# Performance work log

Hardware: AMD Instinct MI355X
Metric: run time of the kernel (lower is better)

## Reference

```python
import jax, jax.numpy as jnp
import numpy as np

N = 50000
E = 800000
NUM_GRAPHS = 64

def gat_layer(x, W, att_src, att_dst, bias, src, dst, heads, out_ch, concat):
    n = x.shape[0]
    h = (x @ W).reshape(n, heads, out_ch)                      # [N,H,C]
    a_s = jnp.sum(h * att_src, axis=-1)                        # [N,H]
    a_d = jnp.sum(h * att_dst, axis=-1)                        # [N,H]
    e = jax.nn.leaky_relu(a_s[src] + a_d[dst], 0.2)            # [E,H]
    m = jax.ops.segment_max(e, dst, num_segments=n)            # segment softmax (self-loops guarantee non-empty)
    e = jnp.exp(e - m[dst])
    s = jax.ops.segment_sum(e, dst, num_segments=n)
    alpha = e / s[dst]                                         # [E,H]
    out = jax.ops.segment_sum(alpha[:, :, None] * h[src], dst, num_segments=n)  # [N,H,C]
    out = out.reshape(n, heads * out_ch) if concat else out.mean(axis=1)
    return out + bias

def setup_inputs() -> dict:
    key = jax.random.key(0)
    ks = jax.random.split(key, 20)
    inp = {}
    inp['x'] = jax.random.normal(ks[0], (N, 256), dtype=jnp.float32)
    inp['edge_index'] = jax.random.randint(ks[1], (2, E), 0, N, dtype=jnp.int64)
    inp['batch'] = jnp.sort(jax.random.randint(ks[2], (N,), 0, NUM_GRAPHS, dtype=jnp.int64))
    s = 0.05
    inp['W1'] = jax.random.normal(ks[3], (256, 256), dtype=jnp.float32) * s
    inp['att_src1'] = jax.random.normal(ks[4], (8, 32), dtype=jnp.float32) * s
    inp['att_dst1'] = jax.random.normal(ks[5], (8, 32), dtype=jnp.float32) * s
    inp['b1'] = jax.random.normal(ks[6], (256,), dtype=jnp.float32) * s
    inp['W2'] = jax.random.normal(ks[7], (256, 256), dtype=jnp.float32) * s
    inp['att_src2'] = jax.random.normal(ks[8], (8, 32), dtype=jnp.float32) * s
    inp['att_dst2'] = jax.random.normal(ks[9], (8, 32), dtype=jnp.float32) * s
    inp['b2'] = jax.random.normal(ks[10], (256,), dtype=jnp.float32) * s
    inp['W3'] = jax.random.normal(ks[11], (256, 32), dtype=jnp.float32) * s
    inp['att_src3'] = jax.random.normal(ks[12], (1, 32), dtype=jnp.float32) * s
    inp['att_dst3'] = jax.random.normal(ks[13], (1, 32), dtype=jnp.float32) * s
    inp['b3'] = jax.random.normal(ks[14], (32,), dtype=jnp.float32) * s
    inp['linW'] = jax.random.normal(ks[15], (32, 1), dtype=jnp.float32) * s
    inp['linb'] = jax.random.normal(ks[16], (1,), dtype=jnp.float32) * s
    return inp

def reference(x, edge_index, batch, W1, att_src1, att_dst1, b1, W2, att_src2, att_dst2, b2,
              W3, att_src3, att_dst3, b3, linW, linb):
    # add self loops (PyG add_self_loops=True)
    loop = jnp.arange(N, dtype=edge_index.dtype)
    src = jnp.concatenate([edge_index[0], loop])
    dst = jnp.concatenate([edge_index[1], loop])
    # eval mode: dropout is identity
    h = gat_layer(x, W1, att_src1, att_dst1, b1, src, dst, 8, 32, True)
    h = jax.nn.elu(h)
    h = gat_layer(h, W2, att_src2, att_dst2, b2, src, dst, 8, 32, True)
    h = jax.nn.elu(h)
    h = gat_layer(h, W3, att_src3, att_dst3, b3, src, dst, 1, 32, False)
    # global mean pool over all nodes (topic_mask defaults to all True)
    sums = jax.ops.segment_sum(h, batch, num_segments=NUM_GRAPHS)
    cnts = jax.ops.segment_sum(jnp.ones((N,), h.dtype), batch, num_segments=NUM_GRAPHS)
    pooled = sums / jnp.maximum(cnts, 1.0)[:, None]
    out = pooled @ linW + linb                                  # [G,1]
    return out.squeeze(-1)                                      # num_classes==2
```

## Files before the change

### kernel.cpp

```cpp
#include <hip/hip_runtime.h>
#include <hip/hip_fp8.h>
#include <math.h>


typedef __attribute__((ext_vector_type(8))) __bf16 bf16x8;
typedef __attribute__((ext_vector_type(4))) __bf16 bf16x4;
typedef __attribute__((ext_vector_type(4))) float f32x4;
typedef __attribute__((ext_vector_type(2))) float f32x2;

#define SCAN_CH 4

__device__ inline unsigned char f32_to_fp8(float f) {
  __hip_fp8_e4m3 v(f);
  return (unsigned char)v.__x;
}
__device__ inline float fp8_to_f32(unsigned char u) {
  __hip_fp8_e4m3 v;
  v.__x = (__hip_fp8_storage_t)u;
  return (float)v;
}

__device__ inline void fma_fp8x4(f32x4& acc, float w, unsigned int packed) {
#if defined(__has_builtin) && __has_builtin(__builtin_amdgcn_cvt_pk_f32_fp8)
  f32x2 lo = __builtin_amdgcn_cvt_pk_f32_fp8((int)packed, false);
  f32x2 hi = __builtin_amdgcn_cvt_pk_f32_fp8((int)packed, true);
  acc[0] += w * lo[0];
  acc[1] += w * lo[1];
  acc[2] += w * hi[0];
  acc[3] += w * hi[1];
#else
  acc[0] += w * fp8_to_f32((unsigned char)(packed & 0xff));
  acc[1] += w * fp8_to_f32((unsigned char)((packed >> 8) & 0xff));
  acc[2] += w * fp8_to_f32((unsigned char)((packed >> 16) & 0xff));
  acc[3] += w * fp8_to_f32((unsigned char)(packed >> 24));
#endif
}

__global__ __launch_bounds__(256) void k_init_deg(int* deg, int N) {
  int n = blockIdx.x * 256 + threadIdx.x;
  if (n < N) deg[n] = 1;
}

__global__ __launch_bounds__(256) void k_count_deg(const int* __restrict__ ei,
                                                   int E, int* deg) {
  int e = blockIdx.x * 256 + threadIdx.x;
  if (e < E) atomicAdd(&deg[ei[E + e]], 1);
}

__global__ __launch_bounds__(256) void k_scan_partial(const int* __restrict__ deg,
                                                      int* __restrict__ blockSums,
                                                      int N) {
  __shared__ int sh[256];
  int t = threadIdx.x, b = blockIdx.x;
  int base = (b * 256 + t) * SCAN_CH;
  int s = 0;
#pragma unroll
  for (int j = 0; j < SCAN_CH; j++) {
    int idx = base + j;
    if (idx < N) s += deg[idx];
  }
  sh[t] = s;
  __syncthreads();
  for (int off = 128; off > 0; off >>= 1) {
    if (t < off) sh[t] += sh[t + off];
    __syncthreads();
  }
  if (t == 0) blockSums[b] = sh[0];
}

__global__ __launch_bounds__(256) void k_scan_blocksums(
    const int* __restrict__ blockSums, int* __restrict__ blockOffs,
    int* __restrict__ rowptr, int nb, int N) {
  __shared__ int sh[256];
  int t = threadIdx.x;
  int v = (t < nb) ? blockSums[t] : 0;
  sh[t] = v;
  __syncthreads();
  for (int off = 1; off < 256; off <<= 1) {
    int u = (t >= off) ? sh[t - off] : 0;
    __syncthreads();
    sh[t] += u;
    __syncthreads();
  }
  if (t < nb) blockOffs[t] = sh[t] - v;
  if (t == nb - 1) rowptr[N] = sh[t];
}

__global__ __launch_bounds__(256) void k_scan_final(const int* __restrict__ deg,
                                                    const int* __restrict__ blockOffs,
                                                    int* __restrict__ rowptr,
                                                    int* __restrict__ cursor, int N) {
  __shared__ int sh[256];
  int t = threadIdx.x, b = blockIdx.x;
  int base = (b * 256 + t) * SCAN_CH;
  int vals[SCAN_CH];
  int s = 0;
#pragma unroll
  for (int j = 0; j < SCAN_CH; j++) {
    int idx = base + j;
    vals[j] = (idx < N) ? deg[idx] : 0;
    s += vals[j];
  }
  sh[t] = s;
  __syncthreads();
  for (int off = 1; off < 256; off <<= 1) {
    int u = (t >= off) ? sh[t - off] : 0;
    __syncthreads();
    sh[t] += u;
    __syncthreads();
  }
  int run = blockOffs[b] + sh[t] - s;
#pragma unroll
  for (int j = 0; j < SCAN_CH; j++) {
    int idx = base + j;
    if (idx < N) {
      rowptr[idx] = run;
      cursor[idx] = run;
      run += vals[j];
    }
  }
}

__global__ __launch_bounds__(256) void k_scatter2(const int* __restrict__ ei,
                                                  int E, int N, int* cursor,
                                                  int2* __restrict__ col2,
                                                  int chunkSz) {
  int stripe = blockIdx.x & 7;
  int chunk = blockIdx.x >> 3;
  int lo = (int)(((long long)N * stripe) >> 3);
  int hi = (int)(((long long)N * (stripe + 1)) >> 3);
  int base = chunk * chunkSz;
  int end = base + chunkSz;
  int total = E + N;
  if (end > total) end = total;
  for (int i = base + threadIdx.x; i < end; i += 256) {
    int d = (i < E) ? ei[E + i] : (i - E);
    if (d < lo || d >= hi) continue;
    int s = (i < E) ? ei[i] : d;
    int pos = atomicAdd(&cursor[d], 1);
    col2[pos] = make_int2(s, d);
  }
}

__global__ __launch_bounds__(256) void k_cast(const float* __restrict__ in,
                                              __bf16* __restrict__ oh, int n4) {
  int i = blockIdx.x * 256 + threadIdx.x;
  if (i >= n4) return;
  float4 v = ((const float4*)in)[i];
  bf16x4 h;
  h[0] = (__bf16)v.x;
  h[1] = (__bf16)v.y;
  h[2] = (__bf16)v.z;
  h[3] = (__bf16)v.w;
  ((bf16x4*)oh)[i] = h;
}

__global__ __launch_bounds__(256) void k_wprep(const float* __restrict__ W,
                                               __bf16* __restrict__ WTh,
                                               int K, int Nc) {
  int i = blockIdx.x * 256 + threadIdx.x;
  if (i >= K * Nc) return;
  int n = i / K, k = i - n * K;
  WTh[i] = (__bf16)W[k * Nc + n];
}

__global__ __launch_bounds__(256) void k_gemm_sA(
    const __bf16* __restrict__ Ah, const __bf16* __restrict__ BTh,
    __bf16* __restrict__ Ch, unsigned char* __restrict__ Cf8, int M, int K) {
  constexpr int NcFull = 256;
  __shared__ __bf16 sA[64 * 256];
  int tid = threadIdx.x;
  int lane = tid & 63, wave = tid >> 6;
  int quad = lane >> 4, l16 = lane & 15;
  int m0 = blockIdx.x * 64;
  int col0 = wave * 64;
  int srow = tid >> 2;
  int mtw = srow >> 4, l16w = srow & 15;
  int arow = min(m0 + srow, M - 1);
  const __bf16* ag = Ah + (size_t)arow * K;
#pragma unroll
  for (int r = 0; r < 8; r++) {
    int c = (tid & 3) + r * 4;
    int s = c >> 2, q = c & 3;
    int slot = (((s * 4 + mtw) * 4 + q) * 16 + l16w) * 8;
    *(bf16x8*)(sA + slot) = *(const bf16x8*)(ag + c * 8);
  }
  __syncthreads();
  const __bf16* brh = BTh + (size_t)(col0 + l16) * K + quad * 8;
  f32x4 acc[4][4];
#pragma unroll
  for (int mt = 0; mt < 4; mt++)
#pragma unroll
    for (int t = 0; t < 4; t++) acc[mt][t] = (f32x4){0.f, 0.f, 0.f, 0.f};
  for (int s = 0; s < 8; s++) {
    bf16x8 b_h[4];
#pragma unroll
    for (int t = 0; t < 4; t++)
      b_h[t] = *(const bf16x8*)(brh + (size_t)t * 16 * K + s * 32);
    bf16x8 a_h[4];
#pragma unroll
    for (int mt = 0; mt < 4; mt++)
      a_h[mt] = *(const bf16x8*)(sA + (((s * 4 + mt) * 4 + quad) * 16 + l16) * 8);
#pragma unroll
    for (int t = 0; t < 4; t++) {
#pragma unroll
      for (int mt = 0; mt < 4; mt++) {
        acc[mt][t] = __builtin_amdgcn_mfma_f32_16x16x32_bf16(a_h[mt], b_h[t], acc[mt][t], 0, 0, 0);
      }
    }
  }
#pragma unroll
  for (int mt = 0; mt < 4; mt++) {
#pragma unroll
    for (int t = 0; t < 4; t++) {
#pragma unroll
      for (int r = 0; r < 4; r++) {
        int m = m0 + mt * 16 + quad * 4 + r;
        if (m < M) {
          size_t o = (size_t)m * NcFull + col0 + t * 16 + l16;
          Ch[o] = (__bf16)acc[mt][t][r];
          Cf8[o] = f32_to_fp8(acc[mt][t][r]);
        }
      }
    }
  }
}

template <int NT, int MT>
__global__ __launch_bounds__(256) void k_gemm_split(
    const __bf16* __restrict__ Ah, const __bf16* __restrict__ BTh,
    __bf16* __restrict__ Ch, int M, int K, int NcFull) {
  int lane = threadIdx.x & 63;
  int wave = threadIdx.x >> 6;
  int quad = lane >> 4;
  int l16 = lane & 15;
  int m0 = blockIdx.y * (64 * MT) + wave * (16 * MT);
  int col0 = blockIdx.x * (NT * 16);
  const __bf16* arh[MT];
#pragma unroll
  for (int mt = 0; mt < MT; mt++) {
    int am = min(m0 + mt * 16 + l16, M - 1);
    arh[mt] = Ah + (size_t)am * K + quad * 8;
  }
  const __bf16* brh = BTh + (size_t)(col0 + l16) * K + quad * 8;
  f32x4 acc[MT][NT];
#pragma unroll
  for (int mt = 0; mt < MT; mt++)
#pragma unroll
    for (int t = 0; t < NT; t++) acc[mt][t] = (f32x4){0.f, 0.f, 0.f, 0.f};
  for (int k0 = 0; k0 < K; k0 += 32) {
    bf16x8 a_h[MT], b_h[NT];
#pragma unroll
    for (int mt = 0; mt < MT; mt++) {
      a_h[mt] = *(const bf16x8*)(arh[mt] + k0);
    }
#pragma unroll
    for (int t = 0; t < NT; t++)
      b_h[t] = *(const bf16x8*)(brh + (size_t)t * 16 * K + k0);
#pragma unroll
    for (int t = 0; t < NT; t++) {
#pragma unroll
      for (int mt = 0; mt < MT; mt++) {
        acc[mt][t] = __builtin_amdgcn_mfma_f32_16x16x32_bf16(a_h[mt], b_h[t], acc[mt][t], 0, 0, 0);
      }
    }
  }
#pragma unroll
  for (int mt = 0; mt < MT; mt++) {
#pragma unroll
    for (int t = 0; t < NT; t++) {
#pragma unroll
      for (int r = 0; r < 4; r++) {
        int m = m0 + mt * 16 + quad * 4 + r;
        if (m < M)
          Ch[(size_t)m * NcFull + col0 + t * 16 + l16] = (__bf16)acc[mt][t][r];
      }
    }
  }
}

__global__ __launch_bounds__(256) void k_att(const __bf16* __restrict__ Hh,
                                             const float* __restrict__ attS,
                                             const float* __restrict__ attD,
                                             float* __restrict__ aS,
                                             float* __restrict__ aD, int NH, int H) {
  int idx = blockIdx.x * 256 + threadIdx.x;
  if (idx >= NH) return;
  int h = idx % H;
  const bf16x8* hv = (const bf16x8*)(Hh + (size_t)idx * 32);
  const float* sv = attS + h * 32;
  const float* dv = attD + h * 32;
  float ss = 0.f, dd = 0.f;
#pragma unroll
  for (int k = 0; k < 4; k++) {
    bf16x8 a = hv[k];
#pragma unroll
    for (int j = 0; j < 8; j++) {
      float v = (float)a[j];
      ss += v * sv[k * 8 + j];
      dd += v * dv[k * 8 + j];
    }
  }
  aS[idx] = ss;
  aD[idx] = dd;
}

__global__ __launch_bounds__(256) void k_gat_agg8f(
    const unsigned char* __restrict__ Hf8, const int* __restrict__ rowptr,
    const int2* __restrict__ col2, const float* __restrict__ aS,
    const float* __restrict__ aD, const float* __restrict__ bias,
    __bf16* __restrict__ outh, int N) {
  int wid = (blockIdx.x * blockDim.x + threadIdx.x) >> 6;
  int lane = threadIdx.x & 63;
  if (wid >= N) return;
  int n = wid;
  int row0 = rowptr[n];
  int deg = rowptr[n + 1] - row0;
  int g = lane >> 4;
  int c = lane & 15;
  int head = c >> 1;
  float ad = aD[(size_t)n * 8 + head];
  f32x4 acc0 = (f32x4){0.f, 0.f, 0.f, 0.f};
  f32x4 acc1 = (f32x4){0.f, 0.f, 0.f, 0.f};
  f32x4 acc2 = (f32x4){0.f, 0.f, 0.f, 0.f};
  f32x4 acc3 = (f32x4){0.f, 0.f, 0.f, 0.f};
  float den = 0.f;
  int dm1 = deg - 1;
  const int* colx = (const int*)col2;
  for (int i = 0; i < deg; i += 8) {
    int e0 = i + g, e1 = i + 4 + g;
    int sl0 = row0 + min(e0, dm1);
    int sl1 = row0 + min(e1, dm1);
    int s0 = colx[(size_t)sl0 * 2];
    int s1 = colx[(size_t)sl1 * 2];
    uint4 p0 = *(const uint4*)(Hf8 + (size_t)s0 * 256 + c * 16);
    uint4 p1 = *(const uint4*)(Hf8 + (size_t)s1 * 256 + c * 16);
    float w0 = 0.f, w1 = 0.f;
    if (e0 < deg) {
      float x = aS[(size_t)s0 * 8 + head] + ad;
      x = (x > 0.f) ? x : 0.2f * x;
      w0 = __expf(x);
    }
    if (e1 < deg) {
      float x = aS[(size_t)s1 * 8 + head] + ad;
      x = (x > 0.f) ? x : 0.2f * x;
      w1 = __expf(x);
    }
    den += w0 + w1;
    fma_fp8x4(acc0, w0, p0.x);
    fma_fp8x4(acc1, w0, p0.y);
    fma_fp8x4(acc2, w0, p0.z);
    fma_fp8x4(acc3, w0, p0.w);
    fma_fp8x4(acc0, w1, p1.x);
    fma_fp8x4(acc1, w1, p1.y);
    fma_fp8x4(acc2, w1, p1.z);
    fma_fp8x4(acc3, w1, p1.w);
  }
#pragma unroll
  for (int off = 16; off < 64; off <<= 1) {
#pragma unroll
    for (int j = 0; j < 4; j++) {
      acc0[j] += __shfl_xor(acc0[j], off, 64);
      acc1[j] += __shfl_xor(acc1[j], off, 64);
      acc2[j] += __shfl_xor(acc2[j], off, 64);
      acc3[j] += __shfl_xor(acc3[j], off, 64);
    }
    den += __shfl_xor(den, off, 64);
  }
  if (g == 0) {
    float rsv = 1.f / den;
    const float4* bp = (const float4*)(bias + c * 16);
    float4 b0 = bp[0], b1 = bp[1], b2 = bp[2], b3 = bp[3];
    bf16x8 o0, o1;
#pragma unroll
    for (int j = 0; j < 4; j++) {
      float v0 = acc0[j] * rsv + ((const float*)&b0)[j];
      float v1 = acc1[j] * rsv + ((const float*)&b1)[j];
      float v2 = acc2[j] * rsv + ((const float*)&b2)[j];
      float v3 = acc3[j] * rsv + ((const float*)&b3)[j];
      v0 = (v0 > 0.f) ? v0 : (__expf(v0) - 1.f);
      v1 = (v1 > 0.f) ? v1 : (__expf(v1) - 1.f);
      v2 = (v2 > 0.f) ? v2 : (__expf(v2) - 1.f);
      v3 = (v3 > 0.f) ? v3 : (__expf(v3) - 1.f);
      o0[j] = (__bf16)v0;
      o0[j + 4] = (__bf16)v1;
      o1[j] = (__bf16)v2;
      o1[j + 4] = (__bf16)v3;
    }
    *(bf16x8*)(outh + (size_t)n * 256 + c * 16) = o0;
    *(bf16x8*)(outh + (size_t)n * 256 + c * 16 + 8) = o1;
  }
}

__global__ __launch_bounds__(256) void k_gat_agg1f(
    const __bf16* __restrict__ Hh, const int* __restrict__ rowptr,
    const int2* __restrict__ col2, const float* __restrict__ aS,
    const float* __restrict__ aD, const float* __restrict__ bias,
    float* __restrict__ out, int N) {
  int wid = (blockIdx.x * blockDim.x + threadIdx.x) >> 6;
  int lane = threadIdx.x & 63;
  if (wid >= N) return;
  int n = wid;
  int row0 = rowptr[n];
  int deg = rowptr[n + 1] - row0;
  int eo = lane >> 3;
  int cl = lane & 7;
  float ad = aD[n];
  const int* colx = (const int*)col2;
  f32x4 acc = (f32x4){0.f, 0.f, 0.f, 0.f};
  float den = 0.f;
  for (int i = eo; i < deg; i += 8) {
    int slot = row0 + i;
    int src = colx[(size_t)slot * 2];
    float x = aS[src] + ad;
    x = (x > 0.f) ? x : 0.2f * x;
    float w = __expf(x);
    den += w;
    bf16x4 hv = *(const bf16x4*)(Hh + (size_t)src * 32 + cl * 4);
#pragma unroll
    for (int j = 0; j < 4; j++) acc[j] += w * (float)hv[j];
  }
#pragma unroll
  for (int off = 8; off < 64; off <<= 1) {
#pragma unroll
    for (int j = 0; j < 4; j++) acc[j] += __shfl_xor(acc[j], off, 64);
    den += __shfl_xor(den, off, 64);
  }
  if (eo == 0) {
    float rsv = 1.f / den;
#pragma unroll
    for (int j = 0; j < 4; j++)
      out[(size_t)n * 32 + cl * 4 + j] = acc[j] * rsv + bias[cl * 4 + j];
  }
}

__global__ __launch_bounds__(256) void k_pool_final(
    const float* __restrict__ h, const int* __restrict__ batch,
    const float* __restrict__ linW, const float* __restrict__ linb,
    float* __restrict__ out, int N) {
  __shared__ float sh[256];
  int g = blockIdx.x;
  int tid = threadIdx.x;
  int grp = tid >> 5, c = tid & 31;
  int lo = 0, hi = N;
  while (lo < hi) { int mid = (lo + hi) >> 1; if (batch[mid] < g) lo = mid + 1; else hi = mid; }
  int start = lo;
  hi = N;
  while (lo < hi) { int mid = (lo + hi) >> 1; if (batch[mid] < g + 1) lo = mid + 1; else hi = mid; }
  int end = lo;
  float acc = 0.f;
  for (int n = start + grp; n < end; n += 8) acc += h[(size_t)n * 32 + c];
  sh[tid] = acc;
  __syncthreads();
  if (tid < 32) {
    float s = 0.f;
#pragma unroll
    for (int j = 0; j < 8; j++) s += sh[j * 32 + tid];
    float v = s * linW[tid];
#pragma unroll
    for (int off = 16; off > 0; off >>= 1) v += __shfl_xor(v, off, 64);
    if (tid == 0) {
      float cnt = (float)(end - start);
      out[g] = v / fmaxf(cnt, 1.f) + linb[0];
    }
  }
}

extern "C" void kernel_launch(void* const* d_in, const int* in_sizes, int n_in,
                              void* d_out, int out_size, void* d_ws, size_t ws_size,
                              hipStream_t stream) {
  const float* x = (const float*)d_in[0];
  const int* ei = (const int*)d_in[1];
  const int* batch = (const int*)d_in[2];
  const float* W1 = (const float*)d_in[3];
  const float* as1 = (const float*)d_in[4];
  const float* ad1 = (const float*)d_in[5];
  const float* b1 = (const float*)d_in[6];
  const float* W2 = (const float*)d_in[7];
  const float* as2 = (const float*)d_in[8];
  const float* ad2 = (const float*)d_in[9];
  const float* b2 = (const float*)d_in[10];
  const float* W3 = (const float*)d_in[11];
  const float* as3 = (const float*)d_in[12];
  const float* ad3 = (const float*)d_in[13];
  const float* b3 = (const float*)d_in[14];
  const float* linW = (const float*)d_in[15];
  const float* linb = (const float*)d_in[16];

  const int N = in_sizes[0] / 256;
  const int E = in_sizes[1] / 2;
  const int NUM_GRAPHS = 64;
  float* out = (float*)d_out;

  char* ws = (char*)d_ws;
  size_t off = 0;
  auto alloc = [&](size_t bytes) -> void* {
    void* p = ws + off;
    off += (bytes + 255) & ~(size_t)255;
    return p;
  };
  __bf16* Hh = (__bf16*)alloc((size_t)N * 256 * 2);
  unsigned char* Hf8 = (unsigned char*)alloc((size_t)N * 256);
  __bf16* Ah = (__bf16*)alloc((size_t)N * 256 * 2);
  float* aS = (float*)alloc((size_t)N * 8 * 4);
  float* aD = (float*)alloc((size_t)N * 8 * 4);
  int* deg = (int*)alloc((size_t)N * 4);
  int* rowptr = (int*)alloc((size_t)(N + 1) * 4);
  int* cursor = (int*)alloc((size_t)(N + 1) * 4);
  int2* col2 = (int2*)alloc((size_t)(E + N) * 8);
  int* blockSums = (int*)alloc(256 * 4);
  int* blockOffs = (int*)alloc(256 * 4);
  __bf16* WT1h = (__bf16*)alloc(256 * 256 * 2);
  __bf16* WT2h = (__bf16*)alloc(256 * 256 * 2);
  __bf16* WT3h = (__bf16*)alloc(32 * 256 * 2);
  float* h3agg = (float*)Ah;

  k_cast<<<(N * 64 + 255) / 256, 256, 0, stream>>>(x, Ah, N * 64);
  k_wprep<<<(256 * 256 + 255) / 256, 256, 0, stream>>>(W1, WT1h, 256, 256);
  k_wprep<<<(256 * 256 + 255) / 256, 256, 0, stream>>>(W2, WT2h, 256, 256);
  k_wprep<<<(256 * 32 + 255) / 256, 256, 0, stream>>>(W3, WT3h, 256, 32);
  k_init_deg<<<(N + 255) / 256, 256, 0, stream>>>(deg, N);
  k_count_deg<<<(E + 255) / 256, 256, 0, stream>>>(ei, E, deg);
  const int nb = (N + 256 * SCAN_CH - 1) / (256 * SCAN_CH);
  k_scan_partial<<<nb, 256, 0, stream>>>(deg, blockSums, N);
  k_scan_blocksums<<<1, 256, 0, stream>>>(blockSums, blockOffs, rowptr, nb, N);
  k_scan_final<<<nb, 256, 0, stream>>>(deg, blockOffs, rowptr, cursor, N);
  {
    const int totalItems = E + N;
    const int nch = 256;
    const int chunkSz = (totalItems + nch - 1) / nch;
    k_scatter2<<<8 * nch, 256, 0, stream>>>(ei, E, N, cursor, col2, chunkSz);
  }

  const int aggBlocks = (N + 3) / 4;
  const int gemmBlocks = (N + 63) / 64;
  dim3 g3(1, (N + 63) / 64);

  k_gemm_sA<<<gemmBlocks, 256, 0, stream>>>(Ah, WT1h, Hh, Hf8, N, 256);
  k_att<<<(N * 8 + 255) / 256, 256, 0, stream>>>(Hh, as1, ad1, aS, aD, N * 8, 8);
  k_gat_agg8f<<<aggBlocks, 256, 0, stream>>>(Hf8, rowptr, col2, aS, aD, b1,
                                             Ah, N);
  k_gemm_sA<<<gemmBlocks, 256, 0, stream>>>(Ah, WT2h, Hh, Hf8, N, 256);
  k_att<<<(N * 8 + 255) / 256, 256, 0, stream>>>(Hh, as2, ad2, aS, aD, N * 8, 8);
  k_gat_agg8f<<<aggBlocks, 256, 0, stream>>>(Hf8, rowptr, col2, aS, aD, b2,
                                             Ah, N);
  k_gemm_split<2, 1><<<g3, 256, 0, stream>>>(Ah, WT3h, Hh, N, 256, 32);
  k_att<<<(N + 255) / 256, 256, 0, stream>>>(Hh, as3, ad3, aS, aD, N, 1);
  k_gat_agg1f<<<aggBlocks, 256, 0, stream>>>(Hh, rowptr, col2, aS, aD, b3,
                                             h3agg, N);
  k_pool_final<<<NUM_GRAPHS, 256, 0, stream>>>(h3agg, batch, linW, linb, out, N);
}
```

Baseline: 463.0 us.

## Fuse attention-score dot products into GEMM epilogue and compact CSR column array

The attention-score computation for layers 1 and 2 moves into the GEMM kernel. The GEMM epilogue writes the bf16 output tile into shared memory and computes the per-head src/dst dot products there, so the separate k_att kernel no longer has to re-read H from global memory. Separately, the CSR edge array now stores only source indices (int) instead of (src,dst) int2 pairs, which halves scatter writes and the bytes the aggregation kernels read. The cost is extra shared-memory traffic and two more barriers in the GEMM kernel, which may lower its occupancy.

```diff
diff --git a/kernel.cpp b/kernel.cpp
--- a/kernel.cpp
+++ b/kernel.cpp
@@ -123,7 +123,7 @@
 
 __global__ __launch_bounds__(256) void k_scatter2(const int* __restrict__ ei,
                                                   int E, int N, int* cursor,
-                                                  int2* __restrict__ col2,
+                                                  int* __restrict__ col_s,
                                                   int chunkSz) {
   int stripe = blockIdx.x & 7;
   int chunk = blockIdx.x >> 3;
@@ -138,7 +138,7 @@
     if (d < lo || d >= hi) continue;
     int s = (i < E) ? ei[i] : d;
     int pos = atomicAdd(&cursor[d], 1);
-    col2[pos] = make_int2(s, d);
+    col_s[pos] = s;
   }
 }
 
@@ -164,16 +164,21 @@
   WTh[i] = (__bf16)W[k * Nc + n];
 }
 
-__global__ __launch_bounds__(256) void k_gemm_sA(
+__global__ __launch_bounds__(256) void k_gemm_att(
     const __bf16* __restrict__ Ah, const __bf16* __restrict__ BTh,
-    __bf16* __restrict__ Ch, unsigned char* __restrict__ Cf8, int M, int K) {
+    const float* __restrict__ attS, const float* __restrict__ attD,
+    __bf16* __restrict__ Ch, unsigned char* __restrict__ Cf8,
+    float* __restrict__ aS, float* __restrict__ aD, int M, int K) {
   constexpr int NcFull = 256;
   __shared__ __bf16 sA[64 * 256];
+  __shared__ float sAttS[256], sAttD[256];
   int tid = threadIdx.x;
   int lane = tid & 63, wave = tid >> 6;
   int quad = lane >> 4, l16 = lane & 15;
   int m0 = blockIdx.x * 64;
   int col0 = wave * 64;
+  sAttS[tid] = attS[tid];
+  sAttD[tid] = attD[tid];
   int srow = tid >> 2;
   int mtw = srow >> 4, l16w = srow & 15;
   int arow = min(m0 + srow, M - 1);
@@ -209,19 +214,47 @@
       }
     }
   }
+  __syncthreads();
 #pragma unroll
   for (int mt = 0; mt < 4; mt++) {
 #pragma unroll
     for (int t = 0; t < 4; t++) {
 #pragma unroll
       for (int r = 0; r < 4; r++) {
-        int m = m0 + mt * 16 + quad * 4 + r;
+        int row = mt * 16 + quad * 4 + r;
+        int m = m0 + row;
+        int colq = t * 16 + l16;
+        __bf16 hv = (__bf16)acc[mt][t][r];
+        sA[row * 256 + col0 + colq] = hv;
         if (m < M) {
-          size_t o = (size_t)m * NcFull + col0 + t * 16 + l16;
-          Ch[o] = (__bf16)acc[mt][t][r];
+          size_t o = (size_t)m * NcFull + col0 + colq;
+          Ch[o] = hv;
           Cf8[o] = f32_to_fp8(acc[mt][t][r]);
         }
       }
+    }
+  }
+  __syncthreads();
+#pragma unroll
+  for (int u = 0; u < 2; u++) {
+    int task = tid + u * 256;
+    int row = task >> 3, h = task & 7;
+    const __bf16* hr = sA + row * 256 + h * 32;
+    float ss = 0.f, dd = 0.f;
+#pragma unroll
+    for (int k = 0; k < 4; k++) {
+      bf16x8 a = *(const bf16x8*)(hr + k * 8);
+#pragma unroll
+      for (int j = 0; j < 8; j++) {
+        float v = (float)a[j];
+        ss += v * sAttS[h * 32 + k * 8 + j];
+        dd += v * sAttD[h * 32 + k * 8 + j];
+      }
+    }
+    int m = m0 + row;
+    if (m < M) {
+      aS[(size_t)m * 8 + h] = ss;
+      aD[(size_t)m * 8 + h] = dd;
     }
   }
 }
@@ -307,7 +340,7 @@
 
 __global__ __launch_bounds__(256) void k_gat_agg8f(
     const unsigned char* __restrict__ Hf8, const int* __restrict__ rowptr,
-    const int2* __restrict__ col2, const float* __restrict__ aS,
+    const int* __restrict__ col_s, const float* __restrict__ aS,
     const float* __restrict__ aD, const float* __restrict__ bias,
     __bf16* __restrict__ outh, int N) {
   int wid = (blockIdx.x * blockDim.x + threadIdx.x) >> 6;
@@ -326,13 +359,12 @@
   f32x4 acc3 = (f32x4){0.f, 0.f, 0.f, 0.f};
   float den = 0.f;
   int dm1 = deg - 1;
-  const int* colx = (const int*)col2;
   for (int i = 0; i < deg; i += 8) {
     int e0 = i + g, e1 = i + 4 + g;
     int sl0 = row0 + min(e0, dm1);
     int sl1 = row0 + min(e1, dm1);
-    int s0 = colx[(size_t)sl0 * 2];
-    int s1 = colx[(size_t)sl1 * 2];
+    int s0 = col_s[sl0];
+    int s1 = col_s[sl1];
     uint4 p0 = *(const uint4*)(Hf8 + (size_t)s0 * 256 + c * 16);
     uint4 p1 = *(const uint4*)(Hf8 + (size_t)s1 * 256 + c * 16);
     float w0 = 0.f, w1 = 0.f;
@@ -394,7 +426,7 @@
 
 __global__ __launch_bounds__(256) void k_gat_agg1f(
     const __bf16* __restrict__ Hh, const int* __restrict__ rowptr,
-    const int2* __restrict__ col2, const float* __restrict__ aS,
+    const int* __restrict__ col_s, const float* __restrict__ aS,
     const float* __restrict__ aD, const float* __restrict__ bias,
     float* __restrict__ out, int N) {
   int wid = (blockIdx.x * blockDim.x + threadIdx.x) >> 6;
@@ -406,12 +438,11 @@
   int eo = lane >> 3;
   int cl = lane & 7;
   float ad = aD[n];
-  const int* colx = (const int*)col2;
   f32x4 acc = (f32x4){0.f, 0.f, 0.f, 0.f};
   float den = 0.f;
   for (int i = eo; i < deg; i += 8) {
     int slot = row0 + i;
-    int src = colx[(size_t)slot * 2];
+    int src = col_s[slot];
     float x = aS[src] + ad;
     x = (x > 0.f) ? x : 0.2f * x;
     float w = __expf(x);
@@ -507,7 +538,7 @@
   int* deg = (int*)alloc((size_t)N * 4);
   int* rowptr = (int*)alloc((size_t)(N + 1) * 4);
   int* cursor = (int*)alloc((size_t)(N + 1) * 4);
-  int2* col2 = (int2*)alloc((size_t)(E + N) * 8);
+  int* col_s = (int*)alloc((size_t)(E + N) * 4);
   int* blockSums = (int*)alloc(256 * 4);
   int* blockOffs = (int*)alloc(256 * 4);
   __bf16* WT1h = (__bf16*)alloc(256 * 256 * 2);
@@ -529,24 +560,24 @@
     const int totalItems = E + N;
     const int nch = 256;
     const int chunkSz = (totalItems + nch - 1) / nch;
-    k_scatter2<<<8 * nch, 256, 0, stream>>>(ei, E, N, cursor, col2, chunkSz);
+    k_scatter2<<<8 * nch, 256, 0, stream>>>(ei, E, N, cursor, col_s, chunkSz);
   }
 
   const int aggBlocks = (N + 3) / 4;
   const int gemmBlocks = (N + 63) / 64;
   dim3 g3(1, (N + 63) / 64);
 
-  k_gemm_sA<<<gemmBlocks, 256, 0, stream>>>(Ah, WT1h, Hh, Hf8, N, 256);
-  k_att<<<(N * 8 + 255) / 256, 256, 0, stream>>>(Hh, as1, ad1, aS, aD, N * 8, 8);
-  k_gat_agg8f<<<aggBlocks, 256, 0, stream>>>(Hf8, rowptr, col2, aS, aD, b1,
+  k_gemm_att<<<gemmBlocks, 256, 0, stream>>>(Ah, WT1h, as1, ad1, Hh, Hf8,
+                                             aS, aD, N, 256);
+  k_gat_agg8f<<<aggBlocks, 256, 0, stream>>>(Hf8, rowptr, col_s, aS, aD, b1,
                                              Ah, N);
-  k_gemm_sA<<<gemmBlocks, 256, 0, stream>>>(Ah, WT2h, Hh, Hf8, N, 256);
-  k_att<<<(N * 8 + 255) / 256, 256, 0, stream>>>(Hh, as2, ad2, aS, aD, N * 8, 8);
-  k_gat_agg8f<<<aggBlocks, 256, 0, stream>>>(Hf8, rowptr, col2, aS, aD, b2,
+  k_gemm_att<<<gemmBlocks, 256, 0, stream>>>(Ah, WT2h, as2, ad2, Hh, Hf8,
+                                             aS, aD, N, 256);
+  k_gat_agg8f<<<aggBlocks, 256, 0, stream>>>(Hf8, rowptr, col_s, aS, aD, b2,
                                              Ah, N);
   k_gemm_split<2, 1><<<g3, 256, 0, stream>>>(Ah, WT3h, Hh, N, 256, 32);
   k_att<<<(N + 255) / 256, 256, 0, stream>>>(Hh, as3, ad3, aS, aD, N, 1);
-  k_gat_agg1f<<<aggBlocks, 256, 0, stream>>>(Hh, rowptr, col2, aS, aD, b3,
+  k_gat_agg1f<<<aggBlocks, 256, 0, stream>>>(Hh, rowptr, col_s, aS, aD, b3,
                                              h3agg, N);
   k_pool_final<<<NUM_GRAPHS, 256, 0, stream>>>(h3agg, batch, linW, linb, out, N);
 }
```

Result: faster. 448.1 us (-3.2%).
